# Performance work log

Measured on AMD Instinct MI355X. Metric: run time of the kernel, lower is better.

Reference implementation:

```python
import jax, jax.numpy as jnp
import numpy as np

B, T, DH, DI, DO = 64, 1024, 512, 1, 1
DT = 1.0
PINH, PCON, G = 0.2, 0.8, 1.5
TAU_LO, TAU_HI = 4.0, 20.0
WOUT_SCL, X_NOISE_SCL = 100.0, 10.0
SEED = 1234


def setup_inputs() -> dict:
    key = jax.random.key(0)
    ks = jax.random.split(key, 7)
    rng = np.random.default_rng(SEED)
    # parameters (match torch init distributions)
    win = jax.random.normal(ks[0], (DH, DI), dtype=jnp.float32)
    m_np = np.eye(DH, dtype=np.float32)
    inh_idxs = rng.choice(DH, size=int(DH * PINH), replace=False)
    m_np[inh_idxs, inh_idxs] = -1.0
    m = jnp.asarray(m_np)
    wout = jax.random.normal(ks[1], (DO, DH), dtype=jnp.float32) / WOUT_SCL
    _w = jax.random.normal(ks[2], (DH, DH), dtype=jnp.float32) * (G / np.sqrt(DH * PCON))
    taus = jax.nn.sigmoid(jax.random.normal(ks[3], (DH, 1), dtype=jnp.float32)) * (TAU_HI - TAU_LO) + TAU_LO
    bias = jnp.zeros((DO, DO), dtype=jnp.float32)
    # forward inputs
    u = jax.random.normal(ks[4], (B, T, DI), dtype=jnp.float32)
    r0 = jax.random.normal(ks[5], (B, DH, 1), dtype=jnp.float32)
    # per-step noise, pre-sampled (torch samples inside the loop)
    noise = jax.random.normal(ks[6], (T, B, DH, 1), dtype=jnp.float32)
    return {"u": u, "r0": r0, "noise": noise, "win": win, "m": m,
            "wout": wout, "_w": _w, "taus": taus, "bias": bias}


def reference(u, r0, noise, win, m, wout, _w, taus, bias):
    # get_w with default nm_signal = identity: w = |_w @ m|
    w = jnp.abs(_w @ m)                      # (dh, dh)
    alpha = DT / taus                        # (dh, 1)
    u_seq = jnp.swapaxes(u, 0, 1)[:, :, None, :]  # (T, B, 1, di)

    def step(x_in, inp):
        u_t, n_t = inp                       # (B,1,di), (B,dh,1)
        r = jax.nn.sigmoid(x_in)             # (B, dh, 1)
        x_new = ((1.0 - alpha) * x_in
                 + alpha * jnp.einsum('hd,bde->bhe', w, r)
                 + jnp.einsum('hi,bie->bhe', win, u_t)
                 + n_t / X_NOISE_SCL)        # (B, dh, 1)
        out = jnp.einsum('oh,bhe->boe', wout, jax.nn.sigmoid(x_new)) + bias  # (B, do, 1)
        out = jnp.swapaxes(out, 1, 2)        # (B, 1, do)
        # faithful to torch: next step receives sigmoid(x_new) as its x
        return jax.nn.sigmoid(x_new), (out, x_new)

    _, (outs, xs) = jax.lax.scan(step, r0, (u_seq, noise))
    outputs = jnp.swapaxes(outs[:, :, 0, :], 0, 1)      # (B, T, do)
    xs_out = jnp.transpose(xs[..., 0], (1, 2, 0))       # (B, dh, T)
    return outputs, xs_out
```

## Files before the change

kernel.cpp:

```cpp
#include <hip/hip_runtime.h>

#define DHN 512
#define TN  1024
#define BN  64
#define CH  16

typedef int int4v __attribute__((ext_vector_type(4)));

static __device__ __forceinline__ float sigm(float x) {
  return 1.0f / (1.0f + __expf(-x));
}

static __device__ __forceinline__ void lds_barrier() {
  __builtin_amdgcn_sched_barrier(0);
  asm volatile("s_waitcnt lgkmcnt(0)\n\ts_barrier" ::: "memory");
  __builtin_amdgcn_sched_barrier(0);
}

#define DPPADD(x, ctrl)                                                    \
  do {                                                                     \
    int _m = __builtin_amdgcn_update_dpp(0, __builtin_bit_cast(int, (x)),  \
                                         (ctrl), 0xF, 0xF, true);          \
    (x) += __builtin_bit_cast(float, _m);                                  \
  } while (0)

static __device__ __forceinline__ float wave_sum_lane63(float x) {
  DPPADD(x, 0x111);
  DPPADD(x, 0x112);
  DPPADD(x, 0x114);
  DPPADD(x, 0x118);
  DPPADD(x, 0x142);
  DPPADD(x, 0x143);
  return x;
}

__global__ __launch_bounds__(512, 2) void k_rnn(
    const float* __restrict__ u, const float* __restrict__ r0,
    const float* __restrict__ noise, const float* __restrict__ win,
    const float* __restrict__ taus, const float* __restrict__ wmat,
    const float* __restrict__ wout, const float* __restrict__ bias,
    float* __restrict__ xs, float* __restrict__ outp) {
  __shared__ float u_lds[TN];
  __shared__ float nz_lds[CH * DHN];
  __shared__ __align__(16) signed char rbuf[2][DHN];
  __shared__ float part_lds[8][CH];
  __shared__ __align__(16) int dsum[DHN];
  __shared__ float qs_lds[DHN];

  const int h    = threadIdx.x;
  const int lane = h & 63;
  const int wv   = h >> 6;
  const int lrow = lane & 15;
  const int lkg  = lane >> 4;
  const int b    = blockIdx.x;
  const float* wrow = wmat + h * DHN;

  float rmax = 1e-30f;
#pragma unroll 8
  for (int k = 0; k < 128; ++k) {
    float4 v = *(const float4*)(wrow + 4 * k);
    rmax = fmaxf(rmax, fabsf(v.x));
    rmax = fmaxf(rmax, fabsf(v.y));
    rmax = fmaxf(rmax, fabsf(v.z));
    rmax = fmaxf(rmax, fabsf(v.w));
  }
  const float qs = 127.0f / rmax;
  qs_lds[h] = qs;

  const float alpha  = 1.0f / taus[h];
  const float beta   = 1.0f - alpha;
  const float win_h  = win[h];
  const float wout_h = wout[h];
  const float bias0  = bias[0];
  const float dscale = rmax * alpha * (1.0f / 16129.0f);
  float s = r0[b * DHN + h];

  for (int i = h; i < TN; i += DHN) u_lds[i] = u[b * TN + i];
  rbuf[0][h] = (signed char)__float2int_rn(sigm(s) * 127.0f);

  __syncthreads();

  int4v wfrag[4][8];
#pragma unroll
  for (int m = 0; m < 4; ++m) {
    const int row = (wv * 4 + m) * 16 + lrow;
    const float qsr = qs_lds[row];
    const float* rp = wmat + (size_t)row * DHN + lkg * 16;
#pragma unroll
    for (int q = 0; q < 8; ++q) {
      const float* cp = rp + q * 64;
      int4v wd;
#pragma unroll
      for (int d = 0; d < 4; ++d) {
        float4 v = *(const float4*)(cp + 4 * d);
        int q0 = min(max(__float2int_rn(fabsf(v.x) * qsr), 0), 127);
        int q1 = min(max(__float2int_rn(fabsf(v.y) * qsr), 0), 127);
        int q2 = min(max(__float2int_rn(fabsf(v.z) * qsr), 0), 127);
        int q3 = min(max(__float2int_rn(fabsf(v.w) * qsr), 0), 127);
        wd[d] = q0 | (q1 << 8) | (q2 << 16) | (q3 << 24);
      }
      wfrag[m][q] = wd;
    }
  }

  const float* np = noise + (size_t)b * DHN + h;
  float* xrow = xs + ((size_t)b * DHN + h) * TN;

  float nreg[CH];
#pragma unroll
  for (int k = 0; k < CH; ++k) nreg[k] = np[(size_t)k * (BN * DHN)];

#pragma unroll 1
  for (int tc = 0; tc < TN; tc += CH) {
    __syncthreads();
    if (tc > 0 && h < CH) {
      float o = bias0;
#pragma unroll
      for (int wq = 0; wq < 8; ++wq) o += part_lds[wq][h];
      outp[b * TN + (tc - CH) + h] = o;
    }
#pragma unroll
    for (int k = 0; k < CH; ++k) nz_lds[k * DHN + h] = nreg[k];
    __syncthreads();
    if (tc + CH < TN) {
#pragma unroll
      for (int k = 0; k < CH; ++k)
        nreg[k] = np[(size_t)(tc + CH + k) * (BN * DHN)];
    }

#pragma unroll 1
    for (int t8 = 0; t8 < CH; t8 += 8) {
      float ua[8];
      *(float4*)&ua[0] = *(const float4*)&u_lds[tc + t8];
      *(float4*)&ua[4] = *(const float4*)&u_lds[tc + t8 + 4];
      float nzv[8];
#pragma unroll
      for (int e = 0; e < 8; ++e) nzv[e] = nz_lds[(t8 + e) * DHN + h];

      float xv[8];
#pragma unroll
      for (int e = 0; e < 8; ++e) {
        const signed char* rbp = &rbuf[e & 1][0];
        int4v bq[8];
#pragma unroll
        for (int q = 0; q < 8; ++q)
          bq[q] = *(const int4v*)(rbp + q * 64 + lkg * 16);

        const int4v zz = {0, 0, 0, 0};
        int4v acc[4];
#pragma unroll
        for (int m = 0; m < 4; ++m) acc[m] = zz;
#pragma unroll
        for (int q = 0; q < 8; ++q) {
#pragma unroll
          for (int m = 0; m < 4; ++m)
            acc[m] = __builtin_amdgcn_mfma_i32_16x16x64_i8(
                wfrag[m][q], bq[q], acc[m], 0, 0, 0);
        }
        if (lrow == 0) {
#pragma unroll
          for (int m = 0; m < 4; ++m)
            *(int4v*)&dsum[wv * 64 + m * 16 + lkg * 4] = acc[m];
        }
        const int dot = dsum[h];
        float x = beta * s + (float)dot * dscale
                + win_h * ua[e] + 0.1f * nzv[e];
        x = fminf(fmaxf(x, -40.0f), 40.0f);
        xv[e] = x;
        float sp = sigm(x);
        rbuf[(e & 1) ^ 1][h] =
            (signed char)__float2int_rn(sigm(sp) * 127.0f);
        s = sp;
        float po = wave_sum_lane63(wout_h * sp);
        if (lane == 63) part_lds[wv][t8 + e] = po;
        lds_barrier();
      }
      float4 p0 = {xv[0], xv[1], xv[2], xv[3]};
      float4 p1 = {xv[4], xv[5], xv[6], xv[7]};
      *(float4*)(xrow + tc + t8)     = p0;
      *(float4*)(xrow + tc + t8 + 4) = p1;
    }
  }
  __syncthreads();
  if (h < CH) {
    float o = bias0;
#pragma unroll
    for (int wq = 0; wq < 8; ++wq) o += part_lds[wq][h];
    outp[b * TN + (TN - CH) + h] = o;
  }
}

extern "C" void kernel_launch(void* const* d_in, const int* in_sizes, int n_in,
                              void* d_out, int out_size, void* d_ws, size_t ws_size,
                              hipStream_t stream) {
  const float* u     = (const float*)d_in[0];
  const float* r0    = (const float*)d_in[1];
  const float* noise = (const float*)d_in[2];
  const float* win   = (const float*)d_in[3];
  const float* wout  = (const float*)d_in[5];
  const float* w_    = (const float*)d_in[6];
  const float* taus  = (const float*)d_in[7];
  const float* bias  = (const float*)d_in[8];

  float* outp = (float*)d_out;
  float* xs   = outp + BN * TN;

  k_rnn<<<BN, DHN, 0, stream>>>(u, r0, noise, win, taus, w_, wout, bias,
                                xs, outp);
}
```

Baseline: 1.234 ms.

## Split recurrent matvec between MFMA waves and sdot4 VALU waves

Waves 0-3 now compute the int8 recurrent matvec over the first half of K for all rows using MFMA, while waves 4-7 handle the second half with sdot4 VALU dot products and readlane broadcasts of r. The two partial sums go to separate LDS arrays and are combined after an added barrier. The aim is to overlap matrix-core and vector-ALU work on each SIMD so the per-step latency of the matvec shrinks. In exchange it adds a second block-wide barrier per timestep. Both register sets (wfrag and wA/wB) sit in one kernel under a launch bound of 2 blocks per CU, which raises register pressure and the risk of spills.

```diff
diff --git a/kernel.cpp b/kernel.cpp
--- a/kernel.cpp
+++ b/kernel.cpp
@@ -4,11 +4,30 @@
 #define TN  1024
 #define BN  64
 #define CH  16
+#define KLO 256
 
 typedef int int4v __attribute__((ext_vector_type(4)));
 
 static __device__ __forceinline__ float sigm(float x) {
   return 1.0f / (1.0f + __expf(-x));
+}
+
+#if defined(__has_builtin)
+#if __has_builtin(__builtin_amdgcn_sdot4)
+#define HAVE_SDOT4 1
+#endif
+#endif
+
+static __device__ __forceinline__ int dot4(int a, int b, int c) {
+#ifdef HAVE_SDOT4
+  return __builtin_amdgcn_sdot4(a, b, c, false);
+#else
+  c += (int)(signed char)(a)       * (int)(signed char)(b);
+  c += (int)(signed char)(a >> 8)  * (int)(signed char)(b >> 8);
+  c += (int)(signed char)(a >> 16) * (int)(signed char)(b >> 16);
+  c += (int)(signed char)(a >> 24) * (int)(signed char)(b >> 24);
+  return c;
+#endif
 }
 
 static __device__ __forceinline__ void lds_barrier() {
@@ -44,7 +63,8 @@
   __shared__ float nz_lds[CH * DHN];
   __shared__ __align__(16) signed char rbuf[2][DHN];
   __shared__ float part_lds[8][CH];
-  __shared__ __align__(16) int dsum[DHN];
+  __shared__ __align__(16) int psumA[DHN];
+  __shared__ int psumB[DHN];
   __shared__ float qs_lds[DHN];
 
   const int h    = threadIdx.x;
@@ -53,6 +73,7 @@
   const int lrow = lane & 15;
   const int lkg  = lane >> 4;
   const int b    = blockIdx.x;
+  const bool mrole = (wv < 4);
   const float* wrow = wmat + h * DHN;
 
   float rmax = 1e-30f;
@@ -80,26 +101,51 @@
 
   __syncthreads();
 
-  int4v wfrag[4][8];
-#pragma unroll
-  for (int m = 0; m < 4; ++m) {
-    const int row = (wv * 4 + m) * 16 + lrow;
-    const float qsr = qs_lds[row];
-    const float* rp = wmat + (size_t)row * DHN + lkg * 16;
-#pragma unroll
-    for (int q = 0; q < 8; ++q) {
-      const float* cp = rp + q * 64;
-      int4v wd;
-#pragma unroll
-      for (int d = 0; d < 4; ++d) {
-        float4 v = *(const float4*)(cp + 4 * d);
-        int q0 = min(max(__float2int_rn(fabsf(v.x) * qsr), 0), 127);
-        int q1 = min(max(__float2int_rn(fabsf(v.y) * qsr), 0), 127);
-        int q2 = min(max(__float2int_rn(fabsf(v.z) * qsr), 0), 127);
-        int q3 = min(max(__float2int_rn(fabsf(v.w) * qsr), 0), 127);
-        wd[d] = q0 | (q1 << 8) | (q2 << 16) | (q3 << 24);
+  int4v wfrag[8][4];
+  int   wA[64], wB[64];
+  if (mrole) {
+#pragma unroll
+    for (int m = 0; m < 8; ++m) {
+      const int row = 128 * wv + 16 * m + lrow;
+      const float qsr = qs_lds[row];
+      const float* rp = wmat + (size_t)row * DHN + lkg * 16;
+#pragma unroll
+      for (int q = 0; q < 4; ++q) {
+        const float* cp = rp + q * 64;
+        int4v wd;
+#pragma unroll
+        for (int d = 0; d < 4; ++d) {
+          float4 v = *(const float4*)(cp + 4 * d);
+          int q0 = min(max(__float2int_rn(fabsf(v.x) * qsr), 0), 127);
+          int q1 = min(max(__float2int_rn(fabsf(v.y) * qsr), 0), 127);
+          int q2 = min(max(__float2int_rn(fabsf(v.z) * qsr), 0), 127);
+          int q3 = min(max(__float2int_rn(fabsf(v.w) * qsr), 0), 127);
+          wd[d] = q0 | (q1 << 8) | (q2 << 16) | (q3 << 24);
+        }
+        wfrag[m][q] = wd;
       }
-      wfrag[m][q] = wd;
+    }
+  } else {
+    const int vw = wv - 4;
+    const int rA = 128 * vw + lane;
+    const int rB = rA + 64;
+    const float qsA = qs_lds[rA], qsB = qs_lds[rB];
+    const float* pA = wmat + (size_t)rA * DHN + KLO;
+    const float* pB = wmat + (size_t)rB * DHN + KLO;
+#pragma unroll
+    for (int j = 0; j < 64; ++j) {
+      float4 va = *(const float4*)(pA + 4 * j);
+      float4 vb = *(const float4*)(pB + 4 * j);
+      int a0 = min(max(__float2int_rn(fabsf(va.x) * qsA), 0), 127);
+      int a1 = min(max(__float2int_rn(fabsf(va.y) * qsA), 0), 127);
+      int a2 = min(max(__float2int_rn(fabsf(va.z) * qsA), 0), 127);
+      int a3 = min(max(__float2int_rn(fabsf(va.w) * qsA), 0), 127);
+      wA[j] = a0 | (a1 << 8) | (a2 << 16) | (a3 << 24);
+      int b0 = min(max(__float2int_rn(fabsf(vb.x) * qsB), 0), 127);
+      int b1 = min(max(__float2int_rn(fabsf(vb.y) * qsB), 0), 127);
+      int b2 = min(max(__float2int_rn(fabsf(vb.z) * qsB), 0), 127);
+      int b3 = min(max(__float2int_rn(fabsf(vb.w) * qsB), 0), 127);
+      wB[j] = b0 | (b1 << 8) | (b2 << 16) | (b3 << 24);
     }
   }
 
@@ -141,28 +187,42 @@
 #pragma unroll
       for (int e = 0; e < 8; ++e) {
         const signed char* rbp = &rbuf[e & 1][0];
-        int4v bq[8];
-#pragma unroll
-        for (int q = 0; q < 8; ++q)
-          bq[q] = *(const int4v*)(rbp + q * 64 + lkg * 16);
-
-        const int4v zz = {0, 0, 0, 0};
-        int4v acc[4];
-#pragma unroll
-        for (int m = 0; m < 4; ++m) acc[m] = zz;
-#pragma unroll
-        for (int q = 0; q < 8; ++q) {
-#pragma unroll
-          for (int m = 0; m < 4; ++m)
-            acc[m] = __builtin_amdgcn_mfma_i32_16x16x64_i8(
-                wfrag[m][q], bq[q], acc[m], 0, 0, 0);
+        if (mrole) {
+          int4v bq[4];
+#pragma unroll
+          for (int q = 0; q < 4; ++q)
+            bq[q] = *(const int4v*)(rbp + q * 64 + lkg * 16);
+          const int4v zz = {0, 0, 0, 0};
+          int4v acc[8];
+#pragma unroll
+          for (int m = 0; m < 8; ++m) acc[m] = zz;
+#pragma unroll
+          for (int q = 0; q < 4; ++q) {
+#pragma unroll
+            for (int m = 0; m < 8; ++m)
+              acc[m] = __builtin_amdgcn_mfma_i32_16x16x64_i8(
+                  wfrag[m][q], bq[q], acc[m], 0, 0, 0);
+          }
+          if (lrow == 0) {
+#pragma unroll
+            for (int m = 0; m < 8; ++m)
+              *(int4v*)&psumA[128 * wv + m * 16 + lkg * 4] = acc[m];
+          }
+        } else {
+          const int vw = wv - 4;
+          const int rv = *(const int*)(rbp + KLO + 4 * lane);
+          int accA = 0, accB = 0;
+#pragma unroll
+          for (int j = 0; j < 64; ++j) {
+            const int rd = __builtin_amdgcn_readlane(rv, j);
+            accA = dot4(wA[j], rd, accA);
+            accB = dot4(wB[j], rd, accB);
+          }
+          psumB[128 * vw + lane]      = accA;
+          psumB[128 * vw + 64 + lane] = accB;
         }
-        if (lrow == 0) {
-#pragma unroll
-          for (int m = 0; m < 4; ++m)
-            *(int4v*)&dsum[wv * 64 + m * 16 + lkg * 4] = acc[m];
-        }
-        const int dot = dsum[h];
+        lds_barrier();
+        const int dot = psumA[h] + psumB[h];
         float x = beta * s + (float)dot * dscale
                 + win_h * ua[e] + 0.1f * nzv[e];
         x = fminf(fmaxf(x, -40.0f), 40.0f);
```

Result: slower. 4.125 ms (+234.2%).

## Split recurrent matvec between MFMA and per-lane sdot4 over the tail columns

Applied to the files above, without the earlier changes.

The K dimension of the int8 recurrent matvec is split. The first 320 columns still go through MFMA with five k-chunks instead of eight. The remaining 192 columns are computed per thread with sdot4, using weights held in registers and r values broadcast via readlane. The aim is to shorten the serial MFMA dependency chain on each timestep by running part of the dot product on the VALU in parallel. The cost is 48 more VGPRs per thread, 48 readlane plus dot4 operations per step, and a larger rbuf.

```diff
diff --git a/kernel.cpp b/kernel.cpp
--- a/kernel.cpp
+++ b/kernel.cpp
@@ -4,11 +4,32 @@
 #define TN  1024
 #define BN  64
 #define CH  16
+#define KLO 320
+#define NQ  5
+#define NJ  48
 
 typedef int int4v __attribute__((ext_vector_type(4)));
 
 static __device__ __forceinline__ float sigm(float x) {
   return 1.0f / (1.0f + __expf(-x));
+}
+
+#if defined(__has_builtin)
+#if __has_builtin(__builtin_amdgcn_sdot4)
+#define HAVE_SDOT4 1
+#endif
+#endif
+
+static __device__ __forceinline__ int dot4(int a, int b, int c) {
+#ifdef HAVE_SDOT4
+  return __builtin_amdgcn_sdot4(a, b, c, false);
+#else
+  c += (int)(signed char)(a)       * (int)(signed char)(b);
+  c += (int)(signed char)(a >> 8)  * (int)(signed char)(b >> 8);
+  c += (int)(signed char)(a >> 16) * (int)(signed char)(b >> 16);
+  c += (int)(signed char)(a >> 24) * (int)(signed char)(b >> 24);
+  return c;
+#endif
 }
 
 static __device__ __forceinline__ void lds_barrier() {
@@ -42,9 +63,9 @@
     float* __restrict__ xs, float* __restrict__ outp) {
   __shared__ float u_lds[TN];
   __shared__ float nz_lds[CH * DHN];
-  __shared__ __align__(16) signed char rbuf[2][DHN];
+  __shared__ __align__(16) signed char rbuf[2][576];
   __shared__ float part_lds[8][CH];
-  __shared__ __align__(16) int dsum[DHN];
+  __shared__ __align__(16) int psum[DHN];
   __shared__ float qs_lds[DHN];
 
   const int h    = threadIdx.x;
@@ -80,16 +101,30 @@
 
   __syncthreads();
 
-  int4v wfrag[4][8];
+  int wd[NJ];
+  {
+    const float* ph = wrow + KLO;
+#pragma unroll
+    for (int j = 0; j < NJ; ++j) {
+      float4 v = *(const float4*)(ph + 4 * j);
+      int q0 = min(max(__float2int_rn(fabsf(v.x) * qs), 0), 127);
+      int q1 = min(max(__float2int_rn(fabsf(v.y) * qs), 0), 127);
+      int q2 = min(max(__float2int_rn(fabsf(v.z) * qs), 0), 127);
+      int q3 = min(max(__float2int_rn(fabsf(v.w) * qs), 0), 127);
+      wd[j] = q0 | (q1 << 8) | (q2 << 16) | (q3 << 24);
+    }
+  }
+
+  int4v wfrag[4][NQ];
 #pragma unroll
   for (int m = 0; m < 4; ++m) {
-    const int row = (wv * 4 + m) * 16 + lrow;
+    const int row = 64 * wv + 16 * m + lrow;
     const float qsr = qs_lds[row];
     const float* rp = wmat + (size_t)row * DHN + lkg * 16;
 #pragma unroll
-    for (int q = 0; q < 8; ++q) {
+    for (int q = 0; q < NQ; ++q) {
       const float* cp = rp + q * 64;
-      int4v wd;
+      int4v wq;
 #pragma unroll
       for (int d = 0; d < 4; ++d) {
         float4 v = *(const float4*)(cp + 4 * d);
@@ -97,9 +132,9 @@
         int q1 = min(max(__float2int_rn(fabsf(v.y) * qsr), 0), 127);
         int q2 = min(max(__float2int_rn(fabsf(v.z) * qsr), 0), 127);
         int q3 = min(max(__float2int_rn(fabsf(v.w) * qsr), 0), 127);
-        wd[d] = q0 | (q1 << 8) | (q2 << 16) | (q3 << 24);
+        wq[d] = q0 | (q1 << 8) | (q2 << 16) | (q3 << 24);
       }
-      wfrag[m][q] = wd;
+      wfrag[m][q] = wq;
     }
   }
 
@@ -141,17 +176,17 @@
 #pragma unroll
       for (int e = 0; e < 8; ++e) {
         const signed char* rbp = &rbuf[e & 1][0];
-        int4v bq[8];
-#pragma unroll
-        for (int q = 0; q < 8; ++q)
+
+        int4v bq[NQ];
+#pragma unroll
+        for (int q = 0; q < NQ; ++q)
           bq[q] = *(const int4v*)(rbp + q * 64 + lkg * 16);
-
         const int4v zz = {0, 0, 0, 0};
         int4v acc[4];
 #pragma unroll
         for (int m = 0; m < 4; ++m) acc[m] = zz;
 #pragma unroll
-        for (int q = 0; q < 8; ++q) {
+        for (int q = 0; q < NQ; ++q) {
 #pragma unroll
           for (int m = 0; m < 4; ++m)
             acc[m] = __builtin_amdgcn_mfma_i32_16x16x64_i8(
@@ -160,9 +195,18 @@
         if (lrow == 0) {
 #pragma unroll
           for (int m = 0; m < 4; ++m)
-            *(int4v*)&dsum[wv * 64 + m * 16 + lkg * 4] = acc[m];
+            *(int4v*)&psum[64 * wv + m * 16 + lkg * 4] = acc[m];
         }
-        const int dot = dsum[h];
+
+        const int rv = *(const int*)(rbp + KLO + 4 * lane);
+        int accL = 0;
+#pragma unroll
+        for (int j = 0; j < NJ; ++j) {
+          const int rd = __builtin_amdgcn_readlane(rv, j);
+          accL = dot4(wd[j], rd, accL);
+        }
+
+        const int dot = psum[h] + accL;
         float x = beta * s + (float)dot * dscale
                 + win_h * ua[e] + 0.1f * nzv[e];
         x = fminf(fmaxf(x, -40.0f), 40.0f);
```

Measured after the change: 1.440 ms. 16.6% more time.
